# Optimization experiments

Hardware: AMD Instinct MI355X
Metric: run time of the kernel (lower is better)

Reference implementation:

```python
import jax, jax.numpy as jnp
import numpy as np

B, T, C, H, S, M = 4, 4096, 1024, 16, 256, 32
D = C // H  # size_head = 64


def setup_inputs() -> dict:
    key = jax.random.key(0)
    ks = jax.random.split(key, 10)
    scale = 1.0 / (C * C)
    return {
        "x_q": jax.random.normal(ks[0], (B, T, C), dtype=jnp.float32),
        "x_r": jax.random.normal(ks[1], (B, T, C), dtype=jnp.float32),
        "y": jax.random.normal(ks[2], (B, T, C), dtype=jnp.float32),
        "Wi": jax.random.normal(ks[3], (C, C), dtype=jnp.float32) * 0.02,
        "bi": jnp.zeros((C,), jnp.float32),
        "Ws": jax.random.normal(ks[4], (S, D), dtype=jnp.float32) * 0.02,
        "bs": jnp.zeros((S,), jnp.float32),
        "temp": jnp.ones((1, H, 1, 1), jnp.float32) / jnp.sqrt(jnp.float32(D)),
        "w_re": jax.random.uniform(ks[5], (H, D, D, M), dtype=jnp.float32) * scale,
        "w_im": jax.random.uniform(ks[6], (H, D, D, M), dtype=jnp.float32) * scale,
        "Wo": jax.random.normal(ks[7], (C, C), dtype=jnp.float32) * 0.02,
        "bo": jnp.zeros((C,), jnp.float32),
    }


def reference(x_q, x_r, y, Wi, bi, Ws, bs, temp, w_re, w_im, Wo, bo):
    b, t, c = x_q.shape
    d = c // H
    # in_proj -> [B, H, T, D]
    tmp = (x_q @ Wi.T + bi).reshape(b, t, H, d).transpose(0, 2, 1, 3)
    # slice logits [B, H, T, S], scaled by learned temperature
    logits = (tmp @ Ws.T + bs) / temp
    # softmax over tokens (n): slice-attention pooling to S virtual points
    z = jnp.einsum('bhnc,bhns->bhsc', tmp, jax.nn.softmax(logits, axis=-2))
    z = z.transpose(0, 1, 3, 2)  # [B, H, D, S]
    n = z.shape[-1]
    z_fft = jnp.fft.rfft(z)  # [B, H, D, S//2+1]
    w = (w_re + 1j * w_im).astype(z_fft.dtype)
    out_m = jnp.einsum('bhix,hiox->bhox', z_fft[..., :M], w)  # [B, H, D, M]
    out_ft = jnp.zeros((b, H, d, n // 2 + 1), dtype=out_m.dtype).at[..., :M].set(out_m)
    out = jnp.fft.irfft(out_ft, n=n)  # [B, H, D, S]
    out = out.transpose(0, 1, 3, 2)  # [B, H, S, D]
    # softmax over slices (g): scatter back to tokens
    out = jnp.einsum('bhgc,bhng->bhnc', out, jax.nn.softmax(logits, axis=-1))
    out = out.transpose(0, 2, 1, 3).reshape(b, t, c)  # merge heads
    return out @ Wo.T + bo
```

## Files before the change

### kernel.cpp

```cpp
#include <hip/hip_runtime.h>
#include <hip/hip_bf16.h>

typedef __attribute__((ext_vector_type(8))) _Float16 half8;
typedef __attribute__((ext_vector_type(4))) _Float16 half4;
typedef __attribute__((ext_vector_type(4))) float f32x4;

#define DEVFN __device__ __forceinline__

constexpr int B_ = 4, T_ = 4096, C_ = 1024, H_ = 16, S_ = 256, M_ = 32, D_ = 64;
constexpr int NT_ = B_ * T_;
constexpr float FSCALE = 65536.0f;
constexpr float TWOPI = 6.283185307179586f;

DEVFN half8 cvt8(const float4 a, const float4 b) {
  half8 h;
  h[0] = (_Float16)a.x; h[1] = (_Float16)a.y; h[2] = (_Float16)a.z; h[3] = (_Float16)a.w;
  h[4] = (_Float16)b.x; h[5] = (_Float16)b.y; h[6] = (_Float16)b.z; h[7] = (_Float16)b.w;
  return h;
}

#define GLD16(gsrc, ldst)                                                        \
  __builtin_amdgcn_global_load_lds(                                              \
      (const __attribute__((address_space(1))) uint32_t*)(gsrc),                 \
      (__attribute__((address_space(3))) uint32_t*)(ldst), 16, 0, 0)

__global__ void k_diag(float* __restrict__ out, float wsz) {
  if (threadIdx.x == 0 && blockIdx.x == 0) out[0] = wsz;
}

__global__ void kw_cvt(const float* __restrict__ src, _Float16* __restrict__ dst, int n) {
  const int i = (blockIdx.x * blockDim.x + threadIdx.x) * 8;
  if (i < n) {
    float4 a = ((const float4*)(src + i))[0];
    float4 b = ((const float4*)(src + i))[1];
    *(half8*)(dst + i) = cvt8(a, b);
  }
}

__global__ void k0_prep(const float* __restrict__ Ws, const float* __restrict__ bs,
                        const float* __restrict__ temp,
                        _Float16* __restrict__ Wsh, float* __restrict__ bsh) {
  const int h = blockIdx.x;
  const int tid = threadIdx.x;
  const float invt = 1.0f / temp[h];
  for (int i = tid; i < S_ * D_; i += 256)
    Wsh[(size_t)h * S_ * D_ + i] = (_Float16)(Ws[i] * invt);
  if (tid < S_) bsh[h * S_ + tid] = bs[tid] * invt;
}

__global__ __launch_bounds__(256) void k1_in_proj(
    const _Float16* __restrict__ Xh, const _Float16* __restrict__ Wih, const float* __restrict__ bi,
    _Float16* __restrict__ tmp_h, _Float16* __restrict__ tmp_hT)
{
  __shared__ _Float16 SMEM[8704];
  _Float16* As = SMEM;
  _Float16* Bs = SMEM + 4096;
  const int tid = threadIdx.x;
  const int orig = blockIdx.y * gridDim.x + blockIdx.x;
  const int wgid = (orig & 7) * 128 + (orig >> 3);
  const int rowBase = (wgid >> 3) * 128;
  const int colBase = (wgid & 7) * 128;
  const int w = tid >> 6, lane = tid & 63;
  const int wr = w >> 1, wc = w & 1;
  const int fr = lane & 15, fg = lane >> 4;
  const int srow0 = w * 16 + (lane >> 2);
  const int srow1 = (4 + w) * 16 + (lane >> 2);
  const int scol  = (lane & 3) * 8;
  const size_t arow0 = (size_t)(rowBase + srow0) * C_ + scol;
  const size_t arow1 = (size_t)(rowBase + srow1) * C_ + scol;
  const size_t brow0 = (size_t)(colBase + srow0) * C_ + scol;
  const size_t brow1 = (size_t)(colBase + srow1) * C_ + scol;
  f32x4 acc[4][4] = {};
  for (int kt = 0; kt < C_; kt += 32) {
    __syncthreads();
    GLD16(Xh  + arow0 + kt, &As[w * 512]);
    GLD16(Xh  + arow1 + kt, &As[(4 + w) * 512]);
    GLD16(Wih + brow0 + kt, &Bs[w * 512]);
    GLD16(Wih + brow1 + kt, &Bs[(4 + w) * 512]);
    __syncthreads();
    half8 a[4], b[4];
#pragma unroll
    for (int i = 0; i < 4; ++i) a[i] = *(const half8*)&As[(wr * 64 + i * 16 + fr) * 32 + fg * 8];
#pragma unroll
    for (int j = 0; j < 4; ++j) b[j] = *(const half8*)&Bs[(wc * 64 + j * 16 + fr) * 32 + fg * 8];
#pragma unroll
    for (int i = 0; i < 4; ++i)
#pragma unroll
      for (int j = 0; j < 4; ++j)
        acc[i][j] = __builtin_amdgcn_mfma_f32_16x16x32_f16(a[i], b[j], acc[i][j], 0, 0, 0);
  }
  const int bb = rowBase >> 12;
  const int tloc = rowBase & (T_ - 1);
#pragma unroll
  for (int i = 0; i < 4; ++i) {
#pragma unroll
    for (int j = 0; j < 4; ++j) {
      const int col = colBase + wc * 64 + j * 16 + fr;
      const int hh = col >> 6, d = col & 63;
      const float bv = bi[col];
      const int t0 = tloc + wr * 64 + i * 16 + fg * 4;
      half4 pk;
#pragma unroll
      for (int r = 0; r < 4; ++r) pk[r] = (_Float16)(acc[i][j][r] + bv);
      *(half4*)&tmp_hT[(((size_t)(bb * H_ + hh)) * D_ + d) * T_ + t0] = pk;
    }
  }
  _Float16 (*Ep)[136] = (_Float16 (*)[136])&SMEM[0];
#pragma unroll
  for (int ph = 0; ph < 2; ++ph) {
    __syncthreads();
    if (wr == ph) {
#pragma unroll
      for (int i = 0; i < 4; ++i)
#pragma unroll
        for (int j = 0; j < 4; ++j) {
          const int col = colBase + wc * 64 + j * 16 + fr;
          const float bv = bi[col];
#pragma unroll
          for (int r = 0; r < 4; ++r)
            Ep[i * 16 + fg * 4 + r][wc * 64 + j * 16 + fr] = (_Float16)(acc[i][j][r] + bv);
        }
    }
    __syncthreads();
#pragma unroll
    for (int h2 = 0; h2 < 2; ++h2) {
      const int hh2 = (colBase >> 6) + h2;
      const size_t base = (((size_t)(bb * H_ + hh2)) * T_ + tloc + ph * 64) * D_;
#pragma unroll
      for (int p = 0; p < 2; ++p) {
        const int idx = p * 256 + tid;
        const int trow = idx >> 3, seg = idx & 7;
        *(half8*)(tmp_h + base + (size_t)trow * D_ + seg * 8) =
            *(const half8*)&Ep[trow][h2 * 64 + seg * 8];
      }
    }
  }
}

__global__ __launch_bounds__(256) void k3_pool(
    const _Float16* __restrict__ tmp_h, const _Float16* __restrict__ tmp_hT,
    const _Float16* __restrict__ Wsh, const float* __restrict__ bsh,
    float* __restrict__ Zpart, float* __restrict__ colsumP)
{
  __shared__ _Float16 Es[256][72];
  const int tid = threadIdx.x;
  const int kc = blockIdx.x;
  const int bh = blockIdx.y;
  const int hh = bh & (H_ - 1);
  const int w = tid >> 6, lane = tid & 63;
  const int fr = lane & 15, fg = lane >> 4;
  const size_t tmpB  = (size_t)bh * T_ * D_;
  const size_t tmpTB = (size_t)bh * D_ * T_;
  const _Float16* WshH = Wsh + (size_t)hh * S_ * D_;
  float bsreg[4];
#pragma unroll
  for (int nj = 0; nj < 4; ++nj) bsreg[nj] = bsh[hh * S_ + w * 64 + nj * 16 + fr];
  f32x4 acc2[4][4] = {};
  float cacc[4] = {0.f, 0.f, 0.f, 0.f};
  half8 pa[2][4];
  half8 pb[2][4];
  {
    const int t0 = kc * 512;
#pragma unroll
    for (int ks = 0; ks < 2; ++ks)
#pragma unroll
      for (int mi = 0; mi < 4; ++mi)
        pa[ks][mi] = *(const half8*)(tmp_h + tmpB + (size_t)(t0 + mi * 16 + fr) * D_ + ks * 32 + fg * 8);
#pragma unroll
    for (int kt = 0; kt < 2; ++kt)
#pragma unroll
      for (int nj = 0; nj < 4; ++nj)
        pb[kt][nj] = *(const half8*)(tmp_hT + tmpTB + (size_t)(nj * 16 + fr) * T_ + t0 + kt * 32 + fg * 8);
  }
  for (int step = 0; step < 8; ++step) {
    const int t0 = kc * 512 + step * 64;
    const int t1 = t0 + 64;
    f32x4 acc1[4][4] = {};
#pragma unroll
    for (int ks = 0; ks < 2; ++ks) {
      half8 b[4];
#pragma unroll
      for (int nj = 0; nj < 4; ++nj)
        b[nj] = *(const half8*)(WshH + (size_t)(w * 64 + nj * 16 + fr) * D_ + ks * 32 + fg * 8);
#pragma unroll
      for (int mi = 0; mi < 4; ++mi)
#pragma unroll
        for (int nj = 0; nj < 4; ++nj)
          acc1[mi][nj] = __builtin_amdgcn_mfma_f32_16x16x32_f16(pa[ks][mi], b[nj], acc1[mi][nj], 0, 0, 0);
    }
    if (step < 7) {
#pragma unroll
      for (int ks = 0; ks < 2; ++ks)
#pragma unroll
        for (int mi = 0; mi < 4; ++mi)
          pa[ks][mi] = *(const half8*)(tmp_h + tmpB + (size_t)(t1 + mi * 16 + fr) * D_ + ks * 32 + fg * 8);
    }
#pragma unroll
    for (int mi = 0; mi < 4; ++mi) {
#pragma unroll
      for (int nj = 0; nj < 4; ++nj) {
        half4 p;
        float csp = 0.f;
#pragma unroll
        for (int r = 0; r < 4; ++r) {
          const float e = __expf(acc1[mi][nj][r] + bsreg[nj]);
          p[r] = (_Float16)e;
          csp += e;
        }
        cacc[nj] += csp;
        *(half4*)&Es[w * 64 + nj * 16 + fr][mi * 16 + fg * 4] = p;
      }
    }
#pragma unroll
    for (int kt = 0; kt < 2; ++kt) {
      half8 a2[4];
#pragma unroll
      for (int mi = 0; mi < 4; ++mi)
        a2[mi] = *(const half8*)&Es[w * 64 + mi * 16 + fr][kt * 32 + fg * 8];
#pragma unroll
      for (int mi = 0; mi < 4; ++mi)
#pragma unroll
        for (int nj = 0; nj < 4; ++nj)
          acc2[mi][nj] = __builtin_amdgcn_mfma_f32_16x16x32_f16(a2[mi], pb[kt][nj], acc2[mi][nj], 0, 0, 0);
    }
    if (step < 7) {
#pragma unroll
      for (int kt = 0; kt < 2; ++kt)
#pragma unroll
        for (int nj = 0; nj < 4; ++nj)
          pb[kt][nj] = *(const half8*)(tmp_hT + tmpTB + (size_t)(nj * 16 + fr) * T_ + t1 + kt * 32 + fg * 8);
    }
  }
#pragma unroll
  for (int nj = 0; nj < 4; ++nj) {
    float v = cacc[nj];
    v += __shfl_xor(v, 16); v += __shfl_xor(v, 32);
    if (fg == 0) colsumP[((size_t)bh * 8 + kc) * S_ + w * 64 + nj * 16 + fr] = v;
  }
#pragma unroll
  for (int mi = 0; mi < 4; ++mi)
#pragma unroll
    for (int nj = 0; nj < 4; ++nj)
#pragma unroll
      for (int r = 0; r < 4; ++r)
        Zpart[(((size_t)bh * 8 + kc) * S_ + w * 64 + mi * 16 + fg * 4 + r) * D_ + nj * 16 + fr]
            = acc2[mi][nj][r];
}

__global__ __launch_bounds__(256) void k4a_dft(
    const float* __restrict__ Zpart, const float* __restrict__ colsumP,
    float* __restrict__ Fre, float* __restrict__ Fim)
{
  __shared__ float zsh[256][17];
  __shared__ float csh[256];
  __shared__ float tc[256], ts[256];
  const int tid = threadIdx.x;
  const int ic = blockIdx.x;
  const int bh = blockIdx.y;
  {
    const float ang = (float)tid * (TWOPI / 256.0f);
    tc[tid] = cosf(ang); ts[tid] = sinf(ang);
    float c = 0.f;
#pragma unroll
    for (int kc = 0; kc < 8; ++kc) c += colsumP[((size_t)bh * 8 + kc) * S_ + tid];
    csh[tid] = c;
  }
  __syncthreads();
  for (int idx = tid; idx < 256 * 16; idx += 256) {
    const int s = idx >> 4, dd = idx & 15;
    float v = 0.f;
#pragma unroll
    for (int kc = 0; kc < 8; ++kc)
      v += Zpart[(((size_t)bh * 8 + kc) * S_ + s) * D_ + ic * 16 + dd];
    zsh[s][dd] = v / csh[s];
  }
  __syncthreads();
  const int ii = tid >> 4;
  const int mh = tid & 15;
#pragma unroll
  for (int q = 0; q < 2; ++q) {
    const int m = mh + 16 * q;
    float re = 0.f, im = 0.f;
    int k = 0;
    for (int s = 0; s < 256; ++s) {
      const float zv = zsh[s][ii];
      re += zv * tc[k];
      im -= zv * ts[k];
      k = (k + m) & 255;
    }
    Fre[((size_t)bh * D_ + ic * 16 + ii) * M_ + m] = re;
    Fim[((size_t)bh * D_ + ic * 16 + ii) * M_ + m] = im;
  }
}

__global__ __launch_bounds__(256) void k4b_mix(
    const float* __restrict__ Fre, const float* __restrict__ Fim,
    const float* __restrict__ w_re, const float* __restrict__ w_im,
    _Float16* __restrict__ fout_T)
{
  __shared__ _Float16 Fsr[4][64][33];
  __shared__ _Float16 Fsi[4][64][33];
  __shared__ float Gpre[2][4][4][32];
  __shared__ float Gpim[2][4][4][32];
  __shared__ float Gre[4][4][32];
  __shared__ float Gim[4][4][32];
  __shared__ float tc[256], ts[256];
  const int tid = threadIdx.x;
  const int oc = blockIdx.x;
  const int h  = blockIdx.y;
  for (int idx = tid; idx < 4 * 64 * 32; idx += 256) {
    const int b = idx >> 11, rem = idx & 2047, i = rem >> 5, m = rem & 31;
    const size_t off = ((size_t)(b * 16 + h) * D_ + i) * M_ + m;
    Fsr[b][i][m] = (_Float16)Fre[off];
    Fsi[b][i][m] = (_Float16)Fim[off];
  }
  {
    const float ang = (float)tid * (TWOPI / 256.0f);
    tc[tid] = cosf(ang); ts[tid] = sinf(ang);
  }
  __syncthreads();
  {
    const int ih = tid >> 7, o = (tid >> 5) & 3, m = tid & 31;
    float gre[4] = {0,0,0,0}, gim[4] = {0,0,0,0};
    for (int i = ih * 32; i < ih * 32 + 32; ++i) {
      const size_t wo = (((size_t)h * D_ + i) * D_ + oc * 4 + o) * M_ + m;
      const float wre = w_re[wo], wim = w_im[wo];
#pragma unroll
      for (int b = 0; b < 4; ++b) {
        const float fre = (float)Fsr[b][i][m], fim = (float)Fsi[b][i][m];
        gre[b] += fre * wre - fim * wim;
        gim[b] += fre * wim + fim * wre;
      }
    }
#pragma unroll
    for (int b = 0; b < 4; ++b) { Gpre[ih][b][o][m] = gre[b]; Gpim[ih][b][o][m] = gim[b]; }
  }
  __syncthreads();
  for (int idx = tid; idx < 512; idx += 256) {
    const int b = idx >> 7, o = (idx >> 5) & 3, m = idx & 31;
    Gre[b][o][m] = Gpre[0][b][o][m] + Gpre[1][b][o][m];
    Gim[b][o][m] = Gpim[0][b][o][m] + Gpim[1][b][o][m];
  }
  __syncthreads();
  {
    const int b = tid >> 6, o = (tid >> 4) & 3, sc = tid & 15;
    for (int s5 = 0; s5 < 16; ++s5) {
      const int s = sc * 16 + s5;
      float v = Gre[b][o][0];
      int km = s;
#pragma unroll
      for (int m = 1; m < 32; ++m) {
        v += 2.0f * (Gre[b][o][m] * tc[km] - Gim[b][o][m] * ts[km]);
        km = (km + s) & 255;
      }
      fout_T[((size_t)(b * 16 + h) * D_ + oc * 4 + o) * S_ + s] = (_Float16)(v * (FSCALE / 256.0f));
    }
  }
}

__global__ __launch_bounds__(256) void k5_scatter(
    const _Float16* __restrict__ Wsh, const float* __restrict__ bsh,
    const _Float16* __restrict__ fout_T, _Float16* __restrict__ tmp_io)
{
  __shared__ _Float16 Fs[64][264];
  __shared__ _Float16 Es[64][264];
  __shared__ float bshl[256];
  const int tid = threadIdx.x;
  const int orig = blockIdx.y * gridDim.x + blockIdx.x;
  const int nidx = (orig & 7) * 64 + (orig >> 3);
  const int bh = nidx >> 3;
  const int tcn = nidx & 7;
  const int hh = bh & (H_ - 1);
  const int w = tid >> 6, lane = tid & 63;
  const int fr = lane & 15, fg = lane >> 4;
  {
    const int row = tid >> 2, c0 = (tid & 3) * 64;
    const _Float16* src = fout_T + (size_t)bh * D_ * S_ + (size_t)row * S_ + c0;
#pragma unroll
    for (int q = 0; q < 8; ++q)
      *(half8*)&Fs[row][c0 + q * 8] = ((const half8*)src)[q];
  }
  bshl[tid] = bsh[hh * S_ + tid];
  __syncthreads();
  const _Float16* WshH = Wsh + (size_t)hh * S_ * D_;
  const size_t tmpB = (size_t)bh * T_ * D_ + (size_t)tcn * 512 * D_;
  const int trow = w * 16 + fr;
  half8 bf0, bf1;
  {
    const _Float16* p = tmp_io + tmpB + (size_t)trow * D_ + fg * 8;
    bf0 = *(const half8*)p;
    bf1 = *(const half8*)(p + 32);
  }
  for (int step = 0; step < 8; ++step) {
    float sumE = 0.f;
    {
      f32x4 acc1[8];
#pragma unroll
      for (int mi = 0; mi < 8; ++mi) acc1[mi] = (f32x4){0.f, 0.f, 0.f, 0.f};
#pragma unroll
      for (int mi = 0; mi < 8; ++mi) {
        const half8 a0 = *(const half8*)(WshH + (size_t)(mi * 16 + fr) * D_ + fg * 8);
        acc1[mi] = __builtin_amdgcn_mfma_f32_16x16x32_f16(a0, bf0, acc1[mi], 0, 0, 0);
      }
#pragma unroll
      for (int mi = 0; mi < 8; ++mi) {
        const half8 a1 = *(const half8*)(WshH + (size_t)(mi * 16 + fr) * D_ + 32 + fg * 8);
        acc1[mi] = __builtin_amdgcn_mfma_f32_16x16x32_f16(a1, bf1, acc1[mi], 0, 0, 0);
      }
#pragma unroll
      for (int mi = 0; mi < 8; ++mi) {
        const float4 bv = *(const float4*)&bshl[mi * 16 + fg * 4];
        float e0 = __expf(acc1[mi][0] + bv.x);
        float e1 = __expf(acc1[mi][1] + bv.y);
        float e2 = __expf(acc1[mi][2] + bv.z);
        float e3 = __expf(acc1[mi][3] + bv.w);
        sumE += (e0 + e1) + (e2 + e3);
        half4 pk;
        pk[0] = (_Float16)e0; pk[1] = (_Float16)e1;
        pk[2] = (_Float16)e2; pk[3] = (_Float16)e3;
        *(half4*)&Es[trow][mi * 16 + fg * 4] = pk;
      }
    }
    {
      f32x4 acc1[8];
#pragma unroll
      for (int mi = 0; mi < 8; ++mi) acc1[mi] = (f32x4){0.f, 0.f, 0.f, 0.f};
#pragma unroll
      for (int mi = 0; mi < 8; ++mi) {
        const half8 a0 = *(const half8*)(WshH + (size_t)((8 + mi) * 16 + fr) * D_ + fg * 8);
        acc1[mi] = __builtin_amdgcn_mfma_f32_16x16x32_f16(a0, bf0, acc1[mi], 0, 0, 0);
      }
#pragma unroll
      for (int mi = 0; mi < 8; ++mi) {
        const half8 a1 = *(const half8*)(WshH + (size_t)((8 + mi) * 16 + fr) * D_ + 32 + fg * 8);
        acc1[mi] = __builtin_amdgcn_mfma_f32_16x16x32_f16(a1, bf1, acc1[mi], 0, 0, 0);
      }
#pragma unroll
      for (int mi = 0; mi < 8; ++mi) {
        const float4 bv = *(const float4*)&bshl[(8 + mi) * 16 + fg * 4];
        float e0 = __expf(acc1[mi][0] + bv.x);
        float e1 = __expf(acc1[mi][1] + bv.y);
        float e2 = __expf(acc1[mi][2] + bv.z);
        float e3 = __expf(acc1[mi][3] + bv.w);
        sumE += (e0 + e1) + (e2 + e3);
        half4 pk;
        pk[0] = (_Float16)e0; pk[1] = (_Float16)e1;
        pk[2] = (_Float16)e2; pk[3] = (_Float16)e3;
        *(half4*)&Es[trow][(8 + mi) * 16 + fg * 4] = pk;
      }
    }
    sumE += __shfl_xor(sumE, 16);
    sumE += __shfl_xor(sumE, 32);
    if (step < 7) {
      const _Float16* p = tmp_io + tmpB + (size_t)((step + 1) * 64 + trow) * D_ + fg * 8;
      bf0 = *(const half8*)p;
      bf1 = *(const half8*)(p + 32);
    }
    f32x4 acc2[4];
#pragma unroll
    for (int nj = 0; nj < 4; ++nj) acc2[nj] = (f32x4){0.f, 0.f, 0.f, 0.f};
#pragma unroll
    for (int ks = 0; ks < 8; ++ks) {
      const half8 ea = *(const half8*)&Es[w * 16 + fr][ks * 32 + fg * 8];
#pragma unroll
      for (int nj = 0; nj < 4; ++nj) {
        const half8 fb = *(const half8*)&Fs[nj * 16 + fr][ks * 32 + fg * 8];
        acc2[nj] = __builtin_amdgcn_mfma_f32_16x16x32_f16(ea, fb, acc2[nj], 0, 0, 0);
      }
    }
    const int tstep0 = tcn * 512 + step * 64;
    {
      float ri[4];
#pragma unroll
      for (int r = 0; r < 4; ++r) ri[r] = 1.0f / __shfl(sumE, fg * 4 + r);
#pragma unroll
      for (int r = 0; r < 4; ++r)
#pragma unroll
        for (int nj = 0; nj < 4; ++nj)
          Es[w * 16 + fg * 4 + r][nj * 16 + fr] = (_Float16)(acc2[nj][r] * ri[r]);
      const int trow8 = lane >> 3, seg = lane & 7;
#pragma unroll
      for (int p = 0; p < 2; ++p) {
        const int rloc = w * 16 + p * 8 + trow8;
        *(half8*)(tmp_io + (size_t)bh * T_ * D_ + (size_t)(tstep0 + rloc) * D_ + seg * 8) =
            *(const half8*)&Es[rloc][seg * 8];
      }
    }
  }
}

__global__ __launch_bounds__(256) void k6_out_proj(
    const _Float16* __restrict__ OT, const _Float16* __restrict__ Woh, const float* __restrict__ bo,
    float* __restrict__ Y)
{
  __shared__ _Float16 As[128 * 32];
  __shared__ _Float16 Bs[128 * 32];
  const int tid = threadIdx.x;
  const int orig = blockIdx.y * gridDim.x + blockIdx.x;
  const int wgid = (orig & 7) * 128 + (orig >> 3);
  const int rowBase = (wgid >> 3) * 128;
  const int colBase = (wgid & 7) * 128;
  const int w = tid >> 6, lane = tid & 63;
  const int wr = w >> 1, wc = w & 1;
  const int fr = lane & 15, fg = lane >> 4;
  const int srow0 = w * 16 + (lane >> 2);
  const int srow1 = (4 + w) * 16 + (lane >> 2);
  const int scol  = (lane & 3) * 8;
  const int g0 = rowBase + srow0, g1 = rowBase + srow1;
  const int bb = g0 >> 12;
  const int t0 = g0 & (T_ - 1), t1 = g1 & (T_ - 1);
  const size_t brow0 = (size_t)(colBase + srow0) * C_ + scol;
  const size_t brow1 = (size_t)(colBase + srow1) * C_ + scol;
  f32x4 acc[4][4] = {};
  for (int kt = 0; kt < C_; kt += 32) {
    const int c0 = kt + scol;
    const int hh0 = c0 >> 6, d0 = c0 & 63;
    __syncthreads();
    GLD16(OT + (((size_t)(bb * H_ + hh0)) * T_ + t0) * D_ + d0, &As[w * 512]);
    GLD16(OT + (((size_t)(bb * H_ + hh0)) * T_ + t1) * D_ + d0, &As[(4 + w) * 512]);
    GLD16(Woh + brow0 + kt, &Bs[w * 512]);
    GLD16(Woh + brow1 + kt, &Bs[(4 + w) * 512]);
    __syncthreads();
    half8 a[4], b[4];
#pragma unroll
    for (int i = 0; i < 4; ++i) a[i] = *(const half8*)&As[(wr * 64 + i * 16 + fr) * 32 + fg * 8];
#pragma unroll
    for (int j = 0; j < 4; ++j) b[j] = *(const half8*)&Bs[(wc * 64 + j * 16 + fr) * 32 + fg * 8];
#pragma unroll
    for (int i = 0; i < 4; ++i)
#pragma unroll
      for (int j = 0; j < 4; ++j)
        acc[i][j] = __builtin_amdgcn_mfma_f32_16x16x32_f16(a[i], b[j], acc[i][j], 0, 0, 0);
  }
#pragma unroll
  for (int i = 0; i < 4; ++i) {
#pragma unroll
    for (int j = 0; j < 4; ++j) {
      const int col = colBase + wc * 64 + j * 16 + fr;
      const float bv = bo[col];
      const int g0o = rowBase + wr * 64 + i * 16 + fg * 4;
#pragma unroll
      for (int r = 0; r < 4; ++r)
        Y[(size_t)(g0o + r) * C_ + col] = acc[i][j][r] * (1.0f / FSCALE) + bv;
    }
  }
}

extern "C" void kernel_launch(void* const* d_in, const int* in_sizes, int n_in,
                              void* d_out, int out_size, void* d_ws, size_t ws_size,
                              hipStream_t stream)
{
  const float* x_q  = (const float*)d_in[0];
  const float* Wi   = (const float*)d_in[3];
  const float* bi   = (const float*)d_in[4];
  const float* Ws   = (const float*)d_in[5];
  const float* bs   = (const float*)d_in[6];
  const float* temp = (const float*)d_in[7];
  const float* w_re = (const float*)d_in[8];
  const float* w_im = (const float*)d_in[9];
  const float* Wo   = (const float*)d_in[10];
  const float* bo   = (const float*)d_in[11];
  float* Y = (float*)d_out;

  char* ws = (char*)d_ws;
  size_t off = 0;
  auto alloc = [&](size_t bytes) { size_t o = off; off += (bytes + 255) & ~(size_t)255; return o; };
  const size_t o_tmp  = alloc((size_t)NT_ * C_ * 2);
  const size_t o_Wsh  = alloc((size_t)H_ * S_ * D_ * 2);
  const size_t o_bsh  = alloc((size_t)H_ * S_ * 4);
  const size_t o_Zp   = alloc((size_t)B_ * H_ * 8 * S_ * D_ * 4);
  const size_t o_colP = alloc((size_t)B_ * H_ * 8 * S_ * 4);
  const size_t o_Fre  = alloc((size_t)B_ * H_ * D_ * M_ * 4);
  const size_t o_Fim  = alloc((size_t)B_ * H_ * D_ * M_ * 4);
  const size_t o_fout = alloc((size_t)B_ * H_ * D_ * S_ * 2);
  const size_t o_Wih  = alloc((size_t)C_ * C_ * 2);
  const size_t o_Woh  = alloc((size_t)C_ * C_ * 2);
  if (off > ws_size) {
    k_diag<<<1, 64, 0, stream>>>(Y, (float)ws_size);
    return;
  }

  _Float16* tmp    = (_Float16*)(ws + o_tmp);
  _Float16* Wsh    = (_Float16*)(ws + o_Wsh);
  float*    bsh    = (float*)(ws + o_bsh);
  float*    Zpart  = (float*)(ws + o_Zp);
  float*    colsumP= (float*)(ws + o_colP);
  float*    Fre    = (float*)(ws + o_Fre);
  float*    Fim    = (float*)(ws + o_Fim);
  _Float16* fout_T = (_Float16*)(ws + o_fout);
  _Float16* Wih    = (_Float16*)(ws + o_Wih);
  _Float16* Woh    = (_Float16*)(ws + o_Woh);
  _Float16* Xh     = (_Float16*)d_out;
  _Float16* tmp_hT = (_Float16*)((char*)d_out + (size_t)NT_ * C_ * 2);

  kw_cvt    <<<dim3(8192),    256, 0, stream>>>(x_q, Xh, NT_ * C_);
  kw_cvt    <<<dim3(512),     256, 0, stream>>>(Wi, Wih, C_ * C_);
  kw_cvt    <<<dim3(512),     256, 0, stream>>>(Wo, Woh, C_ * C_);
  k0_prep   <<<dim3(H_),      256, 0, stream>>>(Ws, bs, temp, Wsh, bsh);
  k1_in_proj<<<dim3(8, 128),  256, 0, stream>>>(Xh, Wih, bi, tmp, tmp_hT);
  k3_pool   <<<dim3(8, B_*H_), 256, 0, stream>>>(tmp, tmp_hT, Wsh, bsh, Zpart, colsumP);
  k4a_dft   <<<dim3(4, B_*H_), 256, 0, stream>>>(Zpart, colsumP, Fre, Fim);
  k4b_mix   <<<dim3(16, H_),   256, 0, stream>>>(Fre, Fim, w_re, w_im, fout_T);
  k5_scatter<<<dim3(8, B_*H_), 256, 0, stream>>>(Wsh, bsh, fout_T, tmp);
  k6_out_proj<<<dim3(8, 128),  256, 0, stream>>>(tmp, Woh, bo, Y);
}
```

Before: 285.3 us.

## Merge prep conversion kernels and widen in_proj GEMM tile to 128x256

The four preprocessing launches (x_q, Wi and Wo fp16 conversion plus Ws/bias temperature scaling) are merged into a single kernel that dispatches on block index. The in-projection GEMM tile grows from 128x128 to 128x256, so each wave holds 4x8 MFMA accumulators and the X tile is reused across twice as many output columns, and the grid drops to 512 blocks. The wider tile needs more LDS and accumulator registers, which may lower occupancy, and the smaller grid gives fewer blocks to spread across the compute units.

```diff
diff --git a/kernel.cpp b/kernel.cpp
--- a/kernel.cpp
+++ b/kernel.cpp
@@ -28,65 +28,81 @@
   if (threadIdx.x == 0 && blockIdx.x == 0) out[0] = wsz;
 }
 
-__global__ void kw_cvt(const float* __restrict__ src, _Float16* __restrict__ dst, int n) {
-  const int i = (blockIdx.x * blockDim.x + threadIdx.x) * 8;
-  if (i < n) {
-    float4 a = ((const float4*)(src + i))[0];
-    float4 b = ((const float4*)(src + i))[1];
-    *(half8*)(dst + i) = cvt8(a, b);
-  }
-}
-
-__global__ void k0_prep(const float* __restrict__ Ws, const float* __restrict__ bs,
-                        const float* __restrict__ temp,
-                        _Float16* __restrict__ Wsh, float* __restrict__ bsh) {
-  const int h = blockIdx.x;
+__global__ void k_prep(const float* __restrict__ xq, const float* __restrict__ Wi,
+                       const float* __restrict__ Wo, const float* __restrict__ Ws,
+                       const float* __restrict__ bs, const float* __restrict__ temp,
+                       _Float16* __restrict__ Xh, _Float16* __restrict__ Wih,
+                       _Float16* __restrict__ Woh, _Float16* __restrict__ Wsh,
+                       float* __restrict__ bsh)
+{
+  const int bid = blockIdx.x;
   const int tid = threadIdx.x;
-  const float invt = 1.0f / temp[h];
-  for (int i = tid; i < S_ * D_; i += 256)
-    Wsh[(size_t)h * S_ * D_ + i] = (_Float16)(Ws[i] * invt);
-  if (tid < S_) bsh[h * S_ + tid] = bs[tid] * invt;
+  if (bid < 8192) {
+    const int i = (bid * 256 + tid) * 8;
+    float4 a = ((const float4*)(xq + i))[0];
+    float4 b = ((const float4*)(xq + i))[1];
+    *(half8*)(Xh + i) = cvt8(a, b);
+  } else if (bid < 8704) {
+    const int i = ((bid - 8192) * 256 + tid) * 8;
+    float4 a = ((const float4*)(Wi + i))[0];
+    float4 b = ((const float4*)(Wi + i))[1];
+    *(half8*)(Wih + i) = cvt8(a, b);
+  } else if (bid < 9216) {
+    const int i = ((bid - 8704) * 256 + tid) * 8;
+    float4 a = ((const float4*)(Wo + i))[0];
+    float4 b = ((const float4*)(Wo + i))[1];
+    *(half8*)(Woh + i) = cvt8(a, b);
+  } else {
+    const int h = bid - 9216;
+    const float invt = 1.0f / temp[h];
+    for (int i = tid; i < S_ * D_; i += 256)
+      Wsh[(size_t)h * S_ * D_ + i] = (_Float16)(Ws[i] * invt);
+    if (tid < S_) bsh[h * S_ + tid] = bs[tid] * invt;
+  }
 }
 
 __global__ __launch_bounds__(256) void k1_in_proj(
     const _Float16* __restrict__ Xh, const _Float16* __restrict__ Wih, const float* __restrict__ bi,
     _Float16* __restrict__ tmp_h, _Float16* __restrict__ tmp_hT)
 {
-  __shared__ _Float16 SMEM[8704];
+  __shared__ _Float16 SMEM[16896];
   _Float16* As = SMEM;
   _Float16* Bs = SMEM + 4096;
   const int tid = threadIdx.x;
-  const int orig = blockIdx.y * gridDim.x + blockIdx.x;
-  const int wgid = (orig & 7) * 128 + (orig >> 3);
-  const int rowBase = (wgid >> 3) * 128;
-  const int colBase = (wgid & 7) * 128;
+  const int orig = blockIdx.x;
+  const int wgid = (orig & 7) * 64 + (orig >> 3);
+  const int rowBase = (wgid >> 2) * 128;
+  const int colBase = (wgid & 3) * 256;
   const int w = tid >> 6, lane = tid & 63;
   const int wr = w >> 1, wc = w & 1;
   const int fr = lane & 15, fg = lane >> 4;
-  const int srow0 = w * 16 + (lane >> 2);
-  const int srow1 = (4 + w) * 16 + (lane >> 2);
-  const int scol  = (lane & 3) * 8;
-  const size_t arow0 = (size_t)(rowBase + srow0) * C_ + scol;
-  const size_t arow1 = (size_t)(rowBase + srow1) * C_ + scol;
-  const size_t brow0 = (size_t)(colBase + srow0) * C_ + scol;
-  const size_t brow1 = (size_t)(colBase + srow1) * C_ + scol;
-  f32x4 acc[4][4] = {};
+  const int lrow = lane >> 2;
+  const int lcol = (lane & 3) * 8;
+  const size_t arow0 = (size_t)(rowBase + w * 16 + lrow) * C_ + lcol;
+  const size_t arow1 = (size_t)(rowBase + (4 + w) * 16 + lrow) * C_ + lcol;
+  const size_t brow0 = (size_t)(colBase + w * 16 + lrow) * C_ + lcol;
+  const size_t brow1 = (size_t)(colBase + (4 + w) * 16 + lrow) * C_ + lcol;
+  const size_t brow2 = (size_t)(colBase + (8 + w) * 16 + lrow) * C_ + lcol;
+  const size_t brow3 = (size_t)(colBase + (12 + w) * 16 + lrow) * C_ + lcol;
+  f32x4 acc[4][8] = {};
   for (int kt = 0; kt < C_; kt += 32) {
     __syncthreads();
     GLD16(Xh  + arow0 + kt, &As[w * 512]);
     GLD16(Xh  + arow1 + kt, &As[(4 + w) * 512]);
     GLD16(Wih + brow0 + kt, &Bs[w * 512]);
     GLD16(Wih + brow1 + kt, &Bs[(4 + w) * 512]);
+    GLD16(Wih + brow2 + kt, &Bs[(8 + w) * 512]);
+    GLD16(Wih + brow3 + kt, &Bs[(12 + w) * 512]);
     __syncthreads();
-    half8 a[4], b[4];
+    half8 a[4], b[8];
 #pragma unroll
     for (int i = 0; i < 4; ++i) a[i] = *(const half8*)&As[(wr * 64 + i * 16 + fr) * 32 + fg * 8];
 #pragma unroll
-    for (int j = 0; j < 4; ++j) b[j] = *(const half8*)&Bs[(wc * 64 + j * 16 + fr) * 32 + fg * 8];
+    for (int j = 0; j < 8; ++j) b[j] = *(const half8*)&Bs[(wc * 128 + j * 16 + fr) * 32 + fg * 8];
 #pragma unroll
     for (int i = 0; i < 4; ++i)
 #pragma unroll
-      for (int j = 0; j < 4; ++j)
+      for (int j = 0; j < 8; ++j)
         acc[i][j] = __builtin_amdgcn_mfma_f32_16x16x32_f16(a[i], b[j], acc[i][j], 0, 0, 0);
   }
   const int bb = rowBase >> 12;
@@ -94,8 +110,8 @@
 #pragma unroll
   for (int i = 0; i < 4; ++i) {
 #pragma unroll
-    for (int j = 0; j < 4; ++j) {
-      const int col = colBase + wc * 64 + j * 16 + fr;
+    for (int j = 0; j < 8; ++j) {
+      const int col = colBase + wc * 128 + j * 16 + fr;
       const int hh = col >> 6, d = col & 63;
       const float bv = bi[col];
       const int t0 = tloc + wr * 64 + i * 16 + fg * 4;
@@ -105,7 +121,7 @@
       *(half4*)&tmp_hT[(((size_t)(bb * H_ + hh)) * D_ + d) * T_ + t0] = pk;
     }
   }
-  _Float16 (*Ep)[136] = (_Float16 (*)[136])&SMEM[0];
+  _Float16 (*Ep)[264] = (_Float16 (*)[264])&SMEM[0];
 #pragma unroll
   for (int ph = 0; ph < 2; ++ph) {
     __syncthreads();
@@ -113,17 +129,17 @@
 #pragma unroll
       for (int i = 0; i < 4; ++i)
 #pragma unroll
-        for (int j = 0; j < 4; ++j) {
-          const int col = colBase + wc * 64 + j * 16 + fr;
-          const float bv = bi[col];
+        for (int j = 0; j < 8; ++j) {
+          const int coloff = wc * 128 + j * 16 + fr;
+          const float bv = bi[colBase + coloff];
 #pragma unroll
           for (int r = 0; r < 4; ++r)
-            Ep[i * 16 + fg * 4 + r][wc * 64 + j * 16 + fr] = (_Float16)(acc[i][j][r] + bv);
+            Ep[i * 16 + fg * 4 + r][coloff] = (_Float16)(acc[i][j][r] + bv);
         }
     }
     __syncthreads();
 #pragma unroll
-    for (int h2 = 0; h2 < 2; ++h2) {
+    for (int h2 = 0; h2 < 4; ++h2) {
       const int hh2 = (colBase >> 6) + h2;
       const size_t base = (((size_t)(bb * H_ + hh2)) * T_ + tloc + ph * 64) * D_;
 #pragma unroll
@@ -593,11 +609,8 @@
   _Float16* Xh     = (_Float16*)d_out;
   _Float16* tmp_hT = (_Float16*)((char*)d_out + (size_t)NT_ * C_ * 2);
 
-  kw_cvt    <<<dim3(8192),    256, 0, stream>>>(x_q, Xh, NT_ * C_);
-  kw_cvt    <<<dim3(512),     256, 0, stream>>>(Wi, Wih, C_ * C_);
-  kw_cvt    <<<dim3(512),     256, 0, stream>>>(Wo, Woh, C_ * C_);
-  k0_prep   <<<dim3(H_),      256, 0, stream>>>(Ws, bs, temp, Wsh, bsh);
-  k1_in_proj<<<dim3(8, 128),  256, 0, stream>>>(Xh, Wih, bi, tmp, tmp_hT);
+  k_prep    <<<dim3(9232),    256, 0, stream>>>(x_q, Wi, Wo, Ws, bs, temp, Xh, Wih, Woh, Wsh, bsh);
+  k1_in_proj<<<dim3(512),     256, 0, stream>>>(Xh, Wih, bi, tmp, tmp_hT);
   k3_pool   <<<dim3(8, B_*H_), 256, 0, stream>>>(tmp, tmp_hT, Wsh, bsh, Zpart, colsumP);
   k4a_dft   <<<dim3(4, B_*H_), 256, 0, stream>>>(Zpart, colsumP, Fre, Fim);
   k4b_mix   <<<dim3(16, H_),   256, 0, stream>>>(Fre, Fim, w_re, w_im, fout_T);
```

Result: slower. 305.7 us (+7.2%).
